# Optimization experiments

Hardware: AMD Instinct MI355X
Metric: run time of the kernel (lower is better)

## Reference

```python
import jax, jax.numpy as jnp
import numpy as np

BATCH, INPUTDIM, OUTDIM, GRIDSIZE = 4096, 256, 256, 64


def setup_inputs() -> dict:
    key = jax.random.key(0)
    k1, k2 = jax.random.split(key)
    x = jax.random.normal(k1, (BATCH, INPUTDIM), dtype=jnp.float32)
    # xavier_uniform over (2, outdim, inputdim, gridsize): fan_in = inputdim*gridsize, fan_out = outdim*gridsize
    fan_in = INPUTDIM * GRIDSIZE
    fan_out = OUTDIM * GRIDSIZE
    limit = float(np.sqrt(6.0 / (fan_in + fan_out)))
    fouriercoeffs = jax.random.uniform(
        k2, (2, OUTDIM, INPUTDIM, GRIDSIZE), dtype=jnp.float32,
        minval=-limit, maxval=limit)
    bias = jnp.zeros((1, OUTDIM), dtype=jnp.float32)
    return {"x": x, "fouriercoeffs": fouriercoeffs, "bias": bias}


def reference(x, fouriercoeffs, bias):
    # x: [B, inputdim]; fouriercoeffs: [2, outdim, inputdim, gridsize]; bias: [1, outdim]
    # gridsize_param is clamp/round'ed to an int in torch -> static = initial_gridsize here.
    G = fouriercoeffs.shape[-1]
    k = jnp.arange(1, G + 1, dtype=x.dtype)        # [G] frequencies 1..G
    xk = x[:, :, None] * k                          # [B, inputdim, G]
    c = jnp.cos(xk)                                 # [B, inputdim, G]
    s = jnp.sin(xk)                                 # [B, inputdim, G]
    # Fused contraction over (inputdim, gridsize) -- avoids the naive
    # [B, outdim, inputdim, gridsize] broadcast tensor of the torch code.
    y = (jnp.einsum('big,oig->bo', c, fouriercoeffs[0])
         + jnp.einsum('big,oig->bo', s, fouriercoeffs[1])
         + bias)                                    # [B, outdim]
    return y
```

## Files before the change

### kernel.cpp

```cpp
#include <hip/hip_runtime.h>
#include <hip/hip_bf16.h>


typedef __attribute__((ext_vector_type(8))) short short8;
typedef __attribute__((ext_vector_type(16))) float f32x16;

#define SPLITK 16
#define ICHUNK (256 / SPLITK)

#define INV2PI 0.15915494309189535f

__device__ __forceinline__ unsigned short f2bf(float f) {
    unsigned u = __builtin_bit_cast(unsigned, f);
    u += 0x7fffu + ((u >> 16) & 1u);
    return (unsigned short)(u >> 16);
}
#if __has_builtin(__builtin_amdgcn_cvt_pk_bf16_f32)
typedef __attribute__((ext_vector_type(2))) __bf16 bf16x2_t;
__device__ __forceinline__ unsigned pkbf16(float a, float b) {
    bf16x2_t v = __builtin_amdgcn_cvt_pk_bf16_f32(a, b);
    return __builtin_bit_cast(unsigned, v);
}
#else
__device__ __forceinline__ unsigned pkbf16(float a, float b) {
    unsigned ua = __builtin_bit_cast(unsigned, a) + 0x8000u;
    unsigned ub = __builtin_bit_cast(unsigned, b) + 0x8000u;
    return __builtin_amdgcn_perm(ub, ua, 0x07060302u);
}
#endif

__device__ __forceinline__ void dbl2(float c, float s, float& co, float& so) {
    float t = c + c;
    co = __builtin_fmaf(t, c, -1.f);
    so = t * s;
}
__device__ __forceinline__ void rot2(float c, float s, float cr, float sr,
                                     float& co, float& so) {
    float t = s * sr;
    co = __builtin_fmaf(c, cr, -t);
    float u = s * cr;
    so = __builtin_fmaf(c, sr, u);
}

__device__ __forceinline__ short8 chain8(float m1, float fm1, float f0) {
    unsigned r[4];
    float vp = fm1, v = f0;
    #pragma unroll
    for (int h = 0; h < 4; ++h) {
        float v1 = __builtin_fmaf(m1, v, -vp);
        r[h] = pkbf16(v, v1);
        float v2 = __builtin_fmaf(m1, v1, -v);
        vp = v1; v = v2;
    }
    uint4 u; u.x = r[0]; u.y = r[1]; u.z = r[2]; u.w = r[3];
    return __builtin_bit_cast(short8, u);
}

__device__ __forceinline__ void async_load16(const void* g, void* l) {
    __builtin_amdgcn_global_load_lds(
        (const __attribute__((address_space(1))) unsigned int*)g,
        (__attribute__((address_space(3))) unsigned int*)l,
        16, 0, 0);
}

__global__ __launch_bounds__(512) void prep_kernel(
    const float* __restrict__ fc, unsigned short* __restrict__ ws2)
{
    __shared__ unsigned pk[512][36];
    const int i = blockIdx.x;
    const int t = threadIdx.x;
    const int rr  = t >> 4;
    const int l16 = t & 15;

    #pragma unroll
    for (int p = 0; p < 16; ++p) {
        int r = p * 32 + rr;
        const float4* src =
            (const float4*)(fc + ((size_t)r * 256 + i) * 64) + l16;
        float4 v = *src;
        pk[r][l16 * 2]     = pkbf16(v.x, v.y);
        pk[r][l16 * 2 + 1] = pkbf16(v.z, v.w);
    }
    __syncthreads();

    #pragma unroll
    for (int gg = 0; gg < 8; ++gg) {
        int gi = gg * 512 + t;
        int sog = gi >> 6, ll = gi & 63;
        int ks = sog >> 3, cb = sog & 7;
        int o  = cb * 32 + (ll & 31);
        int kb = ks * 16 + (ll >> 5) * 8;
        int tt = kb >> 6, g0 = kb & 63;
        int r = tt * 256 + o;
        int c = g0 >> 1;
        uint4 v;
        v.x = pk[r][c]; v.y = pk[r][c + 1];
        v.z = pk[r][c + 2]; v.w = pk[r][c + 3];
        ((uint4*)ws2)[(size_t)i * 4096 + gi] = v;
    }
}

__global__ __launch_bounds__(256) void bias_init(
    const float* __restrict__ bias, float* __restrict__ out)
{
    int idx4 = blockIdx.x * 256 + threadIdx.x;
    ((float4*)out)[idx4] = ((const float4*)bias)[idx4 & 63];
}

__global__ __launch_bounds__(256) void reduce_kernel(
    const unsigned short* __restrict__ pws, const float* __restrict__ bias,
    float* __restrict__ out)
{
    int idx4 = blockIdx.x * 256 + threadIdx.x;
    float4 r = ((const float4*)bias)[idx4 & 63];
    #pragma unroll
    for (int z = 0; z < SPLITK; ++z) {
        ushort4 v = ((const ushort4*)pws)[(size_t)z * 262144 + idx4];
        r.x += __builtin_bit_cast(float, (unsigned)v.x << 16);
        r.y += __builtin_bit_cast(float, (unsigned)v.y << 16);
        r.z += __builtin_bit_cast(float, (unsigned)v.z << 16);
        r.w += __builtin_bit_cast(float, (unsigned)v.w << 16);
    }
    ((float4*)out)[idx4] = r;
}

template <bool USE_WS, bool PARTIAL>
__global__ __launch_bounds__(512, 2) void fkan_gemm(
    const float* __restrict__ x, const float* __restrict__ fc,
    const unsigned short* __restrict__ bws, float* __restrict__ out,
    unsigned short* __restrict__ pws)
{
    __shared__ uint4 Bimg[2][4096];
    __shared__ float xs[ICHUNK][256];

    const int t  = threadIdx.x;
    const int l  = t & 63;
    const int w  = t >> 6;
    const int m32 = l & 31;
    const int h  = l >> 5;

    const int bid = blockIdx.x;
    const int z   = bid & 15;
    const int bx  = bid >> 4;
    const int rowBase = bx * 256;
    const int iBase   = z * ICHUNK;

    f32x16 acc[8];
    #pragma unroll
    for (int a = 0; a < 8; ++a) acc[a] = (f32x16)0.0f;

    auto stageB = [&](int p, int i) {
        if (USE_WS) {
            const uint4* base = (const uint4*)bws + (size_t)i * 4096;
            #pragma unroll
            for (int cc = 0; cc < 8; ++cc) {
                int c = cc * 8 + w;
                async_load16(base + (size_t)c * 64 + l, (void*)(&Bimg[p][c * 64]));
            }
        } else {
            #pragma unroll
            for (int gg = 0; gg < 8; ++gg) {
                int gi  = gg * 512 + t;
                int sog = gi >> 6, ll = gi & 63;
                int ks = sog >> 3, cb = sog & 7;
                int o  = cb * 32 + (ll & 31);
                int kb = ks * 16 + (ll >> 5) * 8;
                int tt = kb >> 6, g0 = kb & 63;
                const float4* p4 = (const float4*)(fc +
                    ((((size_t)tt * 256 + o) * 256 + i) * 64 + g0));
                float4 a = p4[0], b = p4[1];
                uint4 v;
                v.x = pkbf16(a.x, a.y); v.y = pkbf16(a.z, a.w);
                v.z = pkbf16(b.x, b.y); v.w = pkbf16(b.z, b.w);
                Bimg[p][gi] = v;
            }
        }
    };

    stageB(0, iBase);
    {
        const int row = t >> 1;
        const int hf  = t & 1;
        const float4* px =
            (const float4*)(x + (size_t)(rowBase + row) * 256 + iBase) + hf * 2;
        float4 v0 = px[0], v1 = px[1];
        int c0 = hf * 8;
        xs[c0 + 0][row] = v0.x; xs[c0 + 1][row] = v0.y;
        xs[c0 + 2][row] = v0.z; xs[c0 + 3][row] = v0.w;
        xs[c0 + 4][row] = v1.x; xs[c0 + 5][row] = v1.y;
        xs[c0 + 6][row] = v1.z; xs[c0 + 7][row] = v1.w;
    }
    __syncthreads();

    #pragma unroll 1
    for (int ii = 0; ii < ICHUNK; ++ii) {
        const int p = ii & 1;

        if (ii + 1 < ICHUNK) stageB(p ^ 1, iBase + ii + 1);

        short8 aF[8];
        {
            float xv = xs[ii][w * 32 + m32];
            float rev = xv * INV2PI;
            float s1 = __builtin_amdgcn_sinf(rev);
            float c1 = __builtin_amdgcn_cosf(rev);
            const float m1 = c1 + c1;
            float c2, s2, c4, s4, c8, s8, c16, s16;
            dbl2(c1, s1, c2, s2);
            dbl2(c2, s2, c4, s4);
            dbl2(c4, s4, c8, s8);
            dbl2(c8, s8, c16, s16);
            float cB = h ? c8 : 1.f;
            float sB = h ? s8 : 0.f;
            #pragma unroll
            for (int k = 0; k < 4; ++k) {
                float cB1, sB1;
                rot2(cB, sB, c1, s1, cB1, sB1);
                aF[k]     = chain8(m1, cB, cB1);
                aF[4 + k] = chain8(m1, sB, sB1);
                if (k < 3) {
                    float cN, sN;
                    rot2(cB, sB, c16, s16, cN, sN);
                    cB = cN; sB = sN;
                }
            }
        }

        #pragma unroll
        for (int ks = 0; ks < 8; ++ks) {
            short8 bF[8];
            #pragma unroll
            for (int cf = 0; cf < 8; ++cf)
                bF[cf] = __builtin_bit_cast(short8,
                    Bimg[p][(ks * 8 + cf) * 64 + l]);
            #pragma unroll
            for (int cf = 0; cf < 8; ++cf)
                acc[cf] = __builtin_amdgcn_mfma_f32_32x32x16_bf16(
                    aF[ks], bF[cf], acc[cf], 0, 0, 0);
        }

        __syncthreads();
    }

    const int r0 = rowBase + w * 32 + h * 4;
    if (PARTIAL) {
        unsigned short* dst = pws + (size_t)z * (4096u * 256u);
        #pragma unroll
        for (int cf = 0; cf < 8; ++cf)
            #pragma unroll
            for (int e = 0; e < 16; ++e) {
                int rl = (e & 3) + 8 * (e >> 2);
                dst[(size_t)(r0 + rl) * 256 + (cf * 32 + m32)] =
                    f2bf(acc[cf][e]);
            }
    } else {
        #pragma unroll
        for (int cf = 0; cf < 8; ++cf)
            #pragma unroll
            for (int e = 0; e < 16; ++e) {
                int rl = (e & 3) + 8 * (e >> 2);
                atomicAdd(out + (size_t)(r0 + rl) * 256 + (cf * 32 + m32),
                          acc[cf][e]);
            }
    }
}

extern "C" void kernel_launch(void* const* d_in, const int* in_sizes, int n_in,
                              void* d_out, int out_size, void* d_ws, size_t ws_size,
                              hipStream_t stream) {
    const float* x    = (const float*)d_in[0];
    const float* fc   = (const float*)d_in[1];
    const float* bias = (const float*)d_in[2];
    float* out = (float*)d_out;
    unsigned short* bws = (unsigned short*)d_ws;

    const size_t wsCoeff = (size_t)256 * 4096 * 16;
    const size_t wsFull  = wsCoeff + (size_t)SPLITK * 4096 * 256 * 2;
    unsigned short* pws = (unsigned short*)((char*)d_ws + wsCoeff);

    if (ws_size >= wsFull) {
        hipLaunchKernelGGL(prep_kernel, dim3(256), dim3(512), 0, stream, fc, bws);
        hipLaunchKernelGGL((fkan_gemm<true, true>), dim3(256), dim3(512), 0, stream,
                           x, fc, bws, out, pws);
        hipLaunchKernelGGL(reduce_kernel, dim3(1024), dim3(256), 0, stream,
                           pws, bias, out);
    } else if (ws_size >= wsCoeff) {
        hipLaunchKernelGGL(bias_init, dim3(1024), dim3(256), 0, stream, bias, out);
        hipLaunchKernelGGL(prep_kernel, dim3(256), dim3(512), 0, stream, fc, bws);
        hipLaunchKernelGGL((fkan_gemm<true, false>), dim3(256), dim3(512), 0, stream,
                           x, fc, bws, out, pws);
    } else {
        hipLaunchKernelGGL(bias_init, dim3(1024), dim3(256), 0, stream, bias, out);
        hipLaunchKernelGGL((fkan_gemm<false, false>), dim3(256), dim3(512), 0, stream,
                           x, fc, bws, out, pws);
    }
}
```

Baseline: 150.8 us.

## Pipeline B staging in quarter-size slots with fine-grained waitcnt and setprio

The shared B buffer is split into four half-iteration slots, and the async global-to-LDS loads are issued three half-steps ahead. Each step waits with explicit vmcnt counts and raw s_barrier instead of a full __syncthreads, which keeps more loads in flight while MFMAs run. MFMA sections are wrapped in s_setprio to favour the math waves. The hand-counted waitcnt values are fragile: a miscount could read stale LDS, and the raw barriers no longer drain LDS operations.

```diff
diff --git a/kernel.cpp b/kernel.cpp
--- a/kernel.cpp
+++ b/kernel.cpp
@@ -130,7 +130,7 @@
     const unsigned short* __restrict__ bws, float* __restrict__ out,
     unsigned short* __restrict__ pws)
 {
-    __shared__ uint4 Bimg[2][4096];
+    __shared__ uint4 Bflat[8192];
     __shared__ float xs[ICHUNK][256];
 
     const int t  = threadIdx.x;
@@ -149,15 +149,114 @@
     #pragma unroll
     for (int a = 0; a < 8; ++a) acc[a] = (f32x16)0.0f;
 
-    auto stageB = [&](int p, int i) {
-        if (USE_WS) {
-            const uint4* base = (const uint4*)bws + (size_t)i * 4096;
-            #pragma unroll
-            for (int cc = 0; cc < 8; ++cc) {
-                int c = cc * 8 + w;
-                async_load16(base + (size_t)c * 64 + l, (void*)(&Bimg[p][c * 64]));
-            }
-        } else {
+    short8 aF[8];
+
+    auto stageHalf = [&](int slot, int j) {
+        const uint4* base = (const uint4*)bws +
+            (size_t)(iBase + (j >> 1)) * 4096 + (j & 1) * 2048;
+        uint4* dst = Bflat + slot * 2048;
+        #pragma unroll
+        for (int cc = 0; cc < 4; ++cc) {
+            int c = cc * 8 + w;
+            async_load16(base + (size_t)c * 64 + l, (void*)(dst + c * 64));
+        }
+    };
+
+    auto synth = [&](int ii) {
+        float xv = xs[ii][w * 32 + m32];
+        float rev = xv * INV2PI;
+        float s1 = __builtin_amdgcn_sinf(rev);
+        float c1 = __builtin_amdgcn_cosf(rev);
+        const float m1 = c1 + c1;
+        float c2, s2, c4, s4, c8, s8, c16, s16;
+        dbl2(c1, s1, c2, s2);
+        dbl2(c2, s2, c4, s4);
+        dbl2(c4, s4, c8, s8);
+        dbl2(c8, s8, c16, s16);
+        float cB = h ? c8 : 1.f;
+        float sB = h ? s8 : 0.f;
+        #pragma unroll
+        for (int k = 0; k < 4; ++k) {
+            float cB1, sB1;
+            rot2(cB, sB, c1, s1, cB1, sB1);
+            aF[k]     = chain8(m1, cB, cB1);
+            aF[4 + k] = chain8(m1, sB, sB1);
+            if (k < 3) {
+                float cN, sN;
+                rot2(cB, sB, c16, s16, cN, sN);
+                cB = cN; sB = sN;
+            }
+        }
+    };
+
+    auto mfmaHalf = [&](int slot, short8 a0, short8 a1, short8 a2, short8 a3) {
+        const uint4* Bp = Bflat + slot * 2048;
+        short8 av[4] = {a0, a1, a2, a3};
+        #pragma unroll
+        for (int ks = 0; ks < 4; ++ks) {
+            short8 bF[8];
+            #pragma unroll
+            for (int cf = 0; cf < 8; ++cf)
+                bF[cf] = __builtin_bit_cast(short8, Bp[(ks * 8 + cf) * 64 + l]);
+            #pragma unroll
+            for (int cf = 0; cf < 8; ++cf)
+                acc[cf] = __builtin_amdgcn_mfma_f32_32x32x16_bf16(
+                    av[ks], bF[cf], acc[cf], 0, 0, 0);
+        }
+    };
+
+    auto loadXs = [&]() {
+        const int row = t >> 1;
+        const int hf  = t & 1;
+        const float4* px =
+            (const float4*)(x + (size_t)(rowBase + row) * 256 + iBase) + hf * 2;
+        float4 v0 = px[0], v1 = px[1];
+        int c0 = hf * 8;
+        xs[c0 + 0][row] = v0.x; xs[c0 + 1][row] = v0.y;
+        xs[c0 + 2][row] = v0.z; xs[c0 + 3][row] = v0.w;
+        xs[c0 + 4][row] = v1.x; xs[c0 + 5][row] = v1.y;
+        xs[c0 + 6][row] = v1.z; xs[c0 + 7][row] = v1.w;
+    };
+
+    if constexpr (USE_WS) {
+        loadXs();
+        stageHalf(0, 0);
+        stageHalf(1, 1);
+        stageHalf(2, 2);
+        asm volatile("s_waitcnt vmcnt(8) lgkmcnt(0)" ::: "memory");
+        __builtin_amdgcn_s_barrier();
+        asm volatile("" ::: "memory");
+
+        #pragma unroll 1
+        for (int jj = 0; jj < 16; ++jj) {
+            const int j0 = jj * 2;
+
+            if (jj <= 14) stageHalf((j0 + 3) & 3, j0 + 3);
+            synth(jj);
+            __builtin_amdgcn_s_setprio(1);
+            mfmaHalf(j0 & 3, aF[0], aF[1], aF[2], aF[3]);
+            __builtin_amdgcn_s_setprio(0);
+            if (jj < 15) asm volatile("s_waitcnt vmcnt(8)" ::: "memory");
+            else         asm volatile("s_waitcnt vmcnt(0)" ::: "memory");
+            __builtin_amdgcn_s_barrier();
+            asm volatile("" ::: "memory");
+
+            if (jj <= 13) stageHalf((j0 + 4) & 3, j0 + 4);
+            __builtin_amdgcn_s_setprio(1);
+            mfmaHalf((j0 + 1) & 3, aF[4], aF[5], aF[6], aF[7]);
+            __builtin_amdgcn_s_setprio(0);
+            if (jj < 14) {
+                asm volatile("s_waitcnt vmcnt(8)" ::: "memory");
+                __builtin_amdgcn_s_barrier();
+                asm volatile("" ::: "memory");
+            } else if (jj == 14) {
+                asm volatile("s_waitcnt vmcnt(4)" ::: "memory");
+                __builtin_amdgcn_s_barrier();
+                asm volatile("" ::: "memory");
+            }
+        }
+    } else {
+        auto stageBfc = [&](int p, int i) {
             #pragma unroll
             for (int gg = 0; gg < 8; ++gg) {
                 int gi  = gg * 512 + t;
@@ -172,74 +271,21 @@
                 uint4 v;
                 v.x = pkbf16(a.x, a.y); v.y = pkbf16(a.z, a.w);
                 v.z = pkbf16(b.x, b.y); v.w = pkbf16(b.z, b.w);
-                Bimg[p][gi] = v;
-            }
-        }
-    };
-
-    stageB(0, iBase);
-    {
-        const int row = t >> 1;
-        const int hf  = t & 1;
-        const float4* px =
-            (const float4*)(x + (size_t)(rowBase + row) * 256 + iBase) + hf * 2;
-        float4 v0 = px[0], v1 = px[1];
-        int c0 = hf * 8;
-        xs[c0 + 0][row] = v0.x; xs[c0 + 1][row] = v0.y;
-        xs[c0 + 2][row] = v0.z; xs[c0 + 3][row] = v0.w;
-        xs[c0 + 4][row] = v1.x; xs[c0 + 5][row] = v1.y;
-        xs[c0 + 6][row] = v1.z; xs[c0 + 7][row] = v1.w;
-    }
-    __syncthreads();
-
-    #pragma unroll 1
-    for (int ii = 0; ii < ICHUNK; ++ii) {
-        const int p = ii & 1;
-
-        if (ii + 1 < ICHUNK) stageB(p ^ 1, iBase + ii + 1);
-
-        short8 aF[8];
-        {
-            float xv = xs[ii][w * 32 + m32];
-            float rev = xv * INV2PI;
-            float s1 = __builtin_amdgcn_sinf(rev);
-            float c1 = __builtin_amdgcn_cosf(rev);
-            const float m1 = c1 + c1;
-            float c2, s2, c4, s4, c8, s8, c16, s16;
-            dbl2(c1, s1, c2, s2);
-            dbl2(c2, s2, c4, s4);
-            dbl2(c4, s4, c8, s8);
-            dbl2(c8, s8, c16, s16);
-            float cB = h ? c8 : 1.f;
-            float sB = h ? s8 : 0.f;
-            #pragma unroll
-            for (int k = 0; k < 4; ++k) {
-                float cB1, sB1;
-                rot2(cB, sB, c1, s1, cB1, sB1);
-                aF[k]     = chain8(m1, cB, cB1);
-                aF[4 + k] = chain8(m1, sB, sB1);
-                if (k < 3) {
-                    float cN, sN;
-                    rot2(cB, sB, c16, s16, cN, sN);
-                    cB = cN; sB = sN;
-                }
-            }
-        }
-
-        #pragma unroll
-        for (int ks = 0; ks < 8; ++ks) {
-            short8 bF[8];
-            #pragma unroll
-            for (int cf = 0; cf < 8; ++cf)
-                bF[cf] = __builtin_bit_cast(short8,
-                    Bimg[p][(ks * 8 + cf) * 64 + l]);
-            #pragma unroll
-            for (int cf = 0; cf < 8; ++cf)
-                acc[cf] = __builtin_amdgcn_mfma_f32_32x32x16_bf16(
-                    aF[ks], bF[cf], acc[cf], 0, 0, 0);
-        }
-
+                Bflat[p * 4096 + gi] = v;
+            }
+        };
+        stageBfc(0, iBase);
+        loadXs();
         __syncthreads();
+        #pragma unroll 1
+        for (int ii = 0; ii < ICHUNK; ++ii) {
+            const int p = ii & 1;
+            if (ii + 1 < ICHUNK) stageBfc(p ^ 1, iBase + ii + 1);
+            synth(ii);
+            mfmaHalf(p * 2,     aF[0], aF[1], aF[2], aF[3]);
+            mfmaHalf(p * 2 + 1, aF[4], aF[5], aF[6], aF[7]);
+            __syncthreads();
+        }
     }
 
     const int r0 = rowBase + w * 32 + h * 4;
```

Result: no change. 150.5 us (-0.2%).
